# Kernel optimization log

Hardware: AMD Instinct MI355X
Metric: run time of the kernel (lower is better)

## Reference

```python
import jax, jax.numpy as jnp
import numpy as np

IM_H, IM_W = 32, 32
HEADS, HEAD_DIM = 8, 32
IN_DIM = 256
OUT_DIM = 256
N = IM_H * IM_W


def _relative_indices(h, w):
    # replicate torch meshgrid('ij') + flatten logic
    gy, gx = np.meshgrid(np.arange(h), np.arange(w), indexing='ij')
    pos = np.stack([gy.reshape(-1), gx.reshape(-1)])  # (2, n)
    rel = pos[:, :, None] - pos[:, None, :]           # (2, n, n)
    r0 = (rel[0] + (h - 1)) * (2 * w - 1)
    r1 = rel[1] + (w - 1)
    return (r0 + r1).reshape(-1)                      # (n*n,)

_REL_IDX = jnp.asarray(_relative_indices(IM_H, IM_W), dtype=jnp.int32)


def setup_inputs() -> dict:
    key = jax.random.key(0)
    ks = jax.random.split(key, 8)
    d_inner = HEADS * HEAD_DIM
    x = jax.random.normal(ks[0], (16, N, IN_DIM), dtype=jnp.float32)
    Wq = jax.random.normal(ks[1], (IN_DIM, d_inner), dtype=jnp.float32) / np.sqrt(IN_DIM)
    Wk = jax.random.normal(ks[2], (IN_DIM, d_inner), dtype=jnp.float32) / np.sqrt(IN_DIM)
    Wv = jax.random.normal(ks[3], (IN_DIM, d_inner), dtype=jnp.float32) / np.sqrt(IN_DIM)
    bias_table = jax.random.normal(ks[4], ((2 * IM_H - 1) * (2 * IM_W - 1), HEADS), dtype=jnp.float32)
    Wo = jax.random.normal(ks[5], (d_inner, OUT_DIM), dtype=jnp.float32) / np.sqrt(d_inner)
    bo = jax.random.normal(ks[6], (OUT_DIM,), dtype=jnp.float32) * 0.01
    return {"x": x, "Wq": Wq, "Wk": Wk, "Wv": Wv, "bias_table": bias_table, "Wo": Wo, "bo": bo}


def reference(x, Wq, Wk, Wv, bias_table, Wo, bo):
    b, n, _ = x.shape
    scale = HEAD_DIM ** (-0.5)
    # QKV projections -> [b, h, n, d]
    def proj(W):
        return (x @ W).reshape(b, n, HEADS, HEAD_DIM).transpose(0, 2, 1, 3)
    Q, K, V = proj(Wq), proj(Wk), proj(Wv)
    # gathered relative position bias -> [1, h, n, n]
    bias = bias_table[_REL_IDX].reshape(n, n, HEADS).transpose(2, 0, 1)[None]
    scores = jnp.einsum('bhnd,bhmd->bhnm', Q, K) * scale + bias
    attn = jax.nn.softmax(scores, axis=-1)
    out = jnp.einsum('bhnm,bhmd->bhnd', attn, V)
    out = out.transpose(0, 2, 1, 3).reshape(b, n, HEADS * HEAD_DIM)
    return out @ Wo + bo  # dropout is identity in eval mode
```

## Files before the change

### kernel.cpp

```cpp
#include <hip/hip_runtime.h>


using f32x4  = __attribute__((ext_vector_type(4))) float;
using bf16x8 = __attribute__((ext_vector_type(8))) short;

__device__ __forceinline__ short f2bf(float f) {
  union { float f; unsigned u; } v; v.f = f;
  return (short)((v.u + 0x7FFFu + ((v.u >> 16) & 1u)) >> 16);
}
__device__ __forceinline__ f32x4 mfma_k32(bf16x8 a, bf16x8 b, f32x4 c) {
  return __builtin_amdgcn_mfma_f32_16x16x32_bf16(a, b, c, 0, 0, 0);
}
__device__ __forceinline__ int cvt_pk_bf16(float lo, float hi) {
  int r;
  asm("v_cvt_pk_bf16_f32 %0, %1, %2" : "=v"(r) : "v"(lo), "v"(hi));
  return r;
}
__device__ __forceinline__ f32x4 ldb(const float* __restrict__ row, int p) {
  f32x4 v;
  v[0] = row[p]; v[1] = row[p - 1]; v[2] = row[p - 2]; v[3] = row[p - 3];
  return v;
}

#define CSQ 0.25500526817f

__global__ __launch_bounds__(256) void k_prep(const float* __restrict__ Wq,
    const float* __restrict__ Wk, const float* __restrict__ Wv,
    const float* __restrict__ Wo, short* __restrict__ WT,
    const float* __restrict__ bt, float* __restrict__ Tg) {
  int bx = blockIdx.x;
  if (bx < 1024) {
    int wid = bx >> 8, n = bx & 255, k = threadIdx.x;
    const float* W = wid == 0 ? Wq : wid == 1 ? Wk : wid == 2 ? Wv : Wo;
    WT[wid * 65536 + n * 256 + k] = f2bf(W[k * 256 + n]);
  } else {
    int idx = (bx - 1024) * 256 + threadIdx.x;
    int h = idx >> 12, i = idx & 4095;
    if (i < 3969) Tg[idx] = bt[i * 8 + h] * 1.4426950408889634f;
  }
}

__global__ __launch_bounds__(256) void k_qkv(const float* __restrict__ x,
    const short* __restrict__ WT,
    short* __restrict__ Q, short* __restrict__ K, short* __restrict__ Vt) {
  __shared__ short Wlds[2][4096];
  char* lbase = (char*)Wlds;
  const int tid = threadIdx.x;
  const int w = tid >> 6, l = tid & 63, lr = l & 15, lg = l >> 4;
  const int m0 = blockIdx.x * 64;
  const int wi = blockIdx.y;
  const char* Wb = (const char*)(WT + wi * 65536);
  const float* xrow = x + (size_t)(m0 + w * 16 + lr) * 256;
  bf16x8 af[8];
  #pragma unroll
  for (int kc = 0; kc < 8; ++kc) {
    float4 a = *reinterpret_cast<const float4*>(xrow + kc * 32 + lg * 8);
    float4 c = *reinterpret_cast<const float4*>(xrow + kc * 32 + lg * 8 + 4);
    union { int i4[4]; bf16x8 v; } u;
    u.i4[0] = cvt_pk_bf16(a.x, a.y);
    u.i4[1] = cvt_pk_bf16(a.z, a.w);
    u.i4[2] = cvt_pk_bf16(c.x, c.y);
    u.i4[3] = cvt_pk_bf16(c.z, c.w);
    af[kc] = u.v;
  }
  const int Lb0 = tid * 16, Lb1 = 4096 + tid * 16;
  const int P0 = Lb0 ^ (((Lb0 >> 9) & 7) << 4);
  const int P1 = Lb1 ^ (((Lb1 >> 9) & 7) << 4);
  int rdo[8];
  #pragma unroll
  for (int kc = 0; kc < 8; ++kc) {
    int Lg = lr * 512 + kc * 64 + lg * 16;
    rdo[kc] = Lg ^ ((lr & 7) << 4);
  }
  {
    int4 s0 = *reinterpret_cast<const int4*>(Wb + Lb0);
    int4 s1 = *reinterpret_cast<const int4*>(Wb + Lb1);
    *reinterpret_cast<int4*>(lbase + P0) = s0;
    *reinterpret_cast<int4*>(lbase + P1) = s1;
  }
  __syncthreads();
  #pragma unroll 2
  for (int nt = 0; nt < 16; ++nt) {
    const int cur = nt & 1, nxt = cur ^ 1;
    int4 t0, t1;
    if (nt < 15) {
      t0 = *reinterpret_cast<const int4*>(Wb + (nt + 1) * 8192 + Lb0);
      t1 = *reinterpret_cast<const int4*>(Wb + (nt + 1) * 8192 + Lb1);
    }
    f32x4 acc = {0.f, 0.f, 0.f, 0.f};
    #pragma unroll
    for (int kc = 0; kc < 8; ++kc) {
      bf16x8 bfr = *reinterpret_cast<const bf16x8*>(lbase + cur * 8192 + rdo[kc]);
      acc = mfma_k32(af[kc], bfr, acc);
    }
    int colb = nt * 16 + lr;
    int h = colb >> 5, d = colb & 31;
    if (wi == 2) {
      int m = m0 + w * 16 + lg * 4;
      int b = m >> 10, n0 = m & 1023;
      int js = n0 >> 5;
      int lgv = (n0 & 15) >> 2, hi = (n0 >> 4) & 1;
      int jp = lgv * 8 + hi * 4;
      short4 vv;
      vv.x = f2bf(acc[0]); vv.y = f2bf(acc[1]);
      vv.z = f2bf(acc[2]); vv.w = f2bf(acc[3]);
      *reinterpret_cast<short4*>(
          &Vt[(((size_t)(b * 8 + h) * 32 + js) << 10) + d * 32 + jp]) = vv;
    } else {
      #pragma unroll
      for (int r = 0; r < 4; ++r) {
        int m = m0 + w * 16 + lg * 4 + r;
        int b = m >> 10, n = m & 1023;
        short val = (wi == 0) ? f2bf(acc[r] * CSQ) : f2bf(acc[r]);
        if (wi == 0)
          Q[((size_t)(b * 8 + h) * 1024 + n) * 32 + d] = val;
        else
          K[((size_t)(b * 8 + h) * 1024 + n) * 32 + d] = val;
      }
    }
    if (nt < 15) {
      *reinterpret_cast<int4*>(lbase + nxt * 8192 + P0) = t0;
      *reinterpret_cast<int4*>(lbase + nxt * 8192 + P1) = t1;
    }
    __syncthreads();
  }
}

__global__ __launch_bounds__(512) void k_attn(const short* __restrict__ Q,
    const short* __restrict__ K, const short* __restrict__ Vt,
    const float* __restrict__ Tg, short* __restrict__ aout) {
  __shared__ char smraw[18432];
  float* Tlds = (float*)smraw;
  auto mO  = (float(*)[4][4][64])smraw;
  auto mls = (float(*)[2][64])(smraw + 16384);
  const int tid = threadIdx.x, bid = blockIdx.x;
  const int h = bid & 7, qt = (bid >> 3) & 7, b = bid >> 6;
  const float* Th = Tg + (h << 12);
  for (int t = tid; t < 3969; t += 512) Tlds[t] = Th[t];
  __syncthreads();
  const int wg = tid >> 6, l = tid & 63, lr = l & 15, lg = l >> 4;
  const int w = wg & 3, jh = wg >> 2;
  const size_t hoff = (size_t)(b * 8 + h) << 15;
  const short* Qh = Q + hoff;
  const short* Kh = K + hoff;
  const short* Vh = Vt + hoff;
  const int ita = qt * 4 + w;
  const int i0a = ita * 16;
  const int i0b = i0a + 512;
  const int yia = ita >> 1;
  const int pbase = ((ita & 1) << 4) + lr - lg * 4 + 31;
  bf16x8 qfa = *reinterpret_cast<const bf16x8*>(&Qh[(i0a + lr) * 32 + lg * 8]);
  bf16x8 qfb = *reinterpret_cast<const bf16x8*>(&Qh[(i0b + lr) * 32 + lg * 8]);
  f32x4 oa0 = {0.f,0.f,0.f,0.f}, oa1 = {0.f,0.f,0.f,0.f};
  f32x4 ob0 = {0.f,0.f,0.f,0.f}, ob1 = {0.f,0.f,0.f,0.f};
  float lsa = 0.f, lsb = 0.f;
  const int koff0 = lr * 32 + lg * 8, koff1 = (16 + lr) * 32 + lg * 8;
  const int js0 = jh * 16, jsE = js0 + 16;
  bf16x8 kf0 = *reinterpret_cast<const bf16x8*>(&Kh[(js0 << 10) + koff0]);
  bf16x8 kf1 = *reinterpret_cast<const bf16x8*>(&Kh[(js0 << 10) + koff1]);
  bf16x8 vf0 = *reinterpret_cast<const bf16x8*>(&Vh[(js0 << 10) + koff0]);
  bf16x8 vf1 = *reinterpret_cast<const bf16x8*>(&Vh[(js0 << 10) + koff1]);
  #pragma unroll 2
  for (int js = js0; js < jsE; ++js) {
    const int jn = (js + 1 < jsE) ? js + 1 : js;
    bf16x8 nkf0 = *reinterpret_cast<const bf16x8*>(&Kh[(jn << 10) + koff0]);
    bf16x8 nkf1 = *reinterpret_cast<const bf16x8*>(&Kh[(jn << 10) + koff1]);
    bf16x8 nvf0 = *reinterpret_cast<const bf16x8*>(&Vh[(jn << 10) + koff0]);
    bf16x8 nvf1 = *reinterpret_cast<const bf16x8*>(&Vh[(jn << 10) + koff1]);
    const float* TrowA = &Tlds[(yia - js + 31) * 63];
    f32x4 bA0 = ldb(TrowA, pbase);
    f32x4 bA1 = ldb(TrowA, pbase - 16);
    f32x4 bB0 = ldb(TrowA + 1008, pbase);
    f32x4 bB1 = ldb(TrowA + 1008, pbase - 16);
    f32x4 sa0 = mfma_k32(kf0, qfa, bA0);
    f32x4 sa1 = mfma_k32(kf1, qfa, bA1);
    f32x4 sb0 = mfma_k32(kf0, qfb, bB0);
    f32x4 sb1 = mfma_k32(kf1, qfb, bB1);
    float pa0[4], pa1[4], pb0[4], pb1[4];
    #pragma unroll
    for (int r = 0; r < 4; ++r) {
      pa0[r] = __builtin_amdgcn_exp2f(sa0[r]);
      pa1[r] = __builtin_amdgcn_exp2f(sa1[r]);
      pb0[r] = __builtin_amdgcn_exp2f(sb0[r]);
      pb1[r] = __builtin_amdgcn_exp2f(sb1[r]);
      lsa += pa0[r] + pa1[r];
      lsb += pb0[r] + pb1[r];
    }
    union { int i4[4]; bf16x8 v; } pka, pkb;
    pka.i4[0] = cvt_pk_bf16(pa0[0], pa0[1]);
    pka.i4[1] = cvt_pk_bf16(pa0[2], pa0[3]);
    pka.i4[2] = cvt_pk_bf16(pa1[0], pa1[1]);
    pka.i4[3] = cvt_pk_bf16(pa1[2], pa1[3]);
    pkb.i4[0] = cvt_pk_bf16(pb0[0], pb0[1]);
    pkb.i4[1] = cvt_pk_bf16(pb0[2], pb0[3]);
    pkb.i4[2] = cvt_pk_bf16(pb1[0], pb1[1]);
    pkb.i4[3] = cvt_pk_bf16(pb1[2], pb1[3]);
    oa0 = mfma_k32(pka.v, vf0, oa0);
    oa1 = mfma_k32(pka.v, vf1, oa1);
    ob0 = mfma_k32(pkb.v, vf0, ob0);
    ob1 = mfma_k32(pkb.v, vf1, ob1);
    kf0 = nkf0; kf1 = nkf1; vf0 = nvf0; vf1 = nvf1;
  }
  __syncthreads();
  if (jh == 1) {
    #pragma unroll
    for (int r = 0; r < 4; ++r) {
      mO[w][0][r][l] = oa0[r];
      mO[w][1][r][l] = oa1[r];
      mO[w][2][r][l] = ob0[r];
      mO[w][3][r][l] = ob1[r];
    }
    mls[w][0][l] = lsa;
    mls[w][1][l] = lsb;
  }
  __syncthreads();
  if (jh == 0) {
    #pragma unroll
    for (int r = 0; r < 4; ++r) {
      oa0[r] += mO[w][0][r][l];
      oa1[r] += mO[w][1][r][l];
      ob0[r] += mO[w][2][r][l];
      ob1[r] += mO[w][3][r][l];
    }
    lsa += mls[w][0][l];
    lsb += mls[w][1][l];
    {
      float s = lsa + __shfl_xor(lsa, 16);
      s += __shfl_xor(s, 32);
      float inv = 1.0f / s;
      #pragma unroll
      for (int r = 0; r < 4; ++r) {
        float invr = __shfl(inv, lg * 4 + r);
        int n = i0a + lg * 4 + r;
        size_t base = ((size_t)b << 18) + (size_t)n * 256 + h * 32;
        aout[base + lr]      = f2bf(oa0[r] * invr);
        aout[base + 16 + lr] = f2bf(oa1[r] * invr);
      }
      s = lsb + __shfl_xor(lsb, 16);
      s += __shfl_xor(s, 32);
      inv = 1.0f / s;
      #pragma unroll
      for (int r = 0; r < 4; ++r) {
        float invr = __shfl(inv, lg * 4 + r);
        int n = i0b + lg * 4 + r;
        size_t base = ((size_t)b << 18) + (size_t)n * 256 + h * 32;
        aout[base + lr]      = f2bf(ob0[r] * invr);
        aout[base + 16 + lr] = f2bf(ob1[r] * invr);
      }
    }
  }
}

__global__ __launch_bounds__(256) void k_outproj(const short* __restrict__ aout,
    const short* __restrict__ WoT, const float* __restrict__ bo,
    float* __restrict__ out) {
  __shared__ short Wlds[2][4096];
  char* lbase = (char*)Wlds;
  const int tid = threadIdx.x;
  const int w = tid >> 6, l = tid & 63, lr = l & 15, lg = l >> 4;
  const int m0 = blockIdx.x * 64;
  const char* Wb = (const char*)WoT;
  const short* arow = aout + (size_t)(m0 + w * 16 + lr) * 256;
  bf16x8 af[8];
  #pragma unroll
  for (int kc = 0; kc < 8; ++kc)
    af[kc] = *reinterpret_cast<const bf16x8*>(arow + kc * 32 + lg * 8);
  const int Lb0 = tid * 16, Lb1 = 4096 + tid * 16;
  const int P0 = Lb0 ^ (((Lb0 >> 9) & 7) << 4);
  const int P1 = Lb1 ^ (((Lb1 >> 9) & 7) << 4);
  int rdo[8];
  #pragma unroll
  for (int kc = 0; kc < 8; ++kc) {
    int Lg = lr * 512 + kc * 64 + lg * 16;
    rdo[kc] = Lg ^ ((lr & 7) << 4);
  }
  {
    int4 s0 = *reinterpret_cast<const int4*>(Wb + Lb0);
    int4 s1 = *reinterpret_cast<const int4*>(Wb + Lb1);
    *reinterpret_cast<int4*>(lbase + P0) = s0;
    *reinterpret_cast<int4*>(lbase + P1) = s1;
  }
  __syncthreads();
  #pragma unroll 2
  for (int nt = 0; nt < 16; ++nt) {
    const int cur = nt & 1, nxt = cur ^ 1;
    int4 t0, t1;
    if (nt < 15) {
      t0 = *reinterpret_cast<const int4*>(Wb + (nt + 1) * 8192 + Lb0);
      t1 = *reinterpret_cast<const int4*>(Wb + (nt + 1) * 8192 + Lb1);
    }
    f32x4 acc = {0.f, 0.f, 0.f, 0.f};
    #pragma unroll
    for (int kc = 0; kc < 8; ++kc) {
      bf16x8 bfr = *reinterpret_cast<const bf16x8*>(lbase + cur * 8192 + rdo[kc]);
      acc = mfma_k32(af[kc], bfr, acc);
    }
    int colb = nt * 16 + lr;
    float bias = bo[colb];
    #pragma unroll
    for (int r = 0; r < 4; ++r) {
      int m = m0 + w * 16 + lg * 4 + r;
      out[(size_t)m * 256 + colb] = acc[r] + bias;
    }
    if (nt < 15) {
      *reinterpret_cast<int4*>(lbase + nxt * 8192 + P0) = t0;
      *reinterpret_cast<int4*>(lbase + nxt * 8192 + P1) = t1;
    }
    __syncthreads();
  }
}

extern "C" void kernel_launch(void* const* d_in, const int* in_sizes, int n_in,
                              void* d_out, int out_size, void* d_ws, size_t ws_size,
                              hipStream_t stream) {
  const float* x  = (const float*)d_in[0];
  const float* Wq = (const float*)d_in[1];
  const float* Wk = (const float*)d_in[2];
  const float* Wv = (const float*)d_in[3];
  const float* bt = (const float*)d_in[4];
  const float* Wo = (const float*)d_in[5];
  const float* bo = (const float*)d_in[6];
  float* out = (float*)d_out;
  char* ws = (char*)d_ws;
  short* WT   = (short*)ws;
  short* Qs   = (short*)(ws + 512 * 1024);
  short* Ks   = Qs + 4194304;
  short* Vts  = Ks + 4194304;
  short* aout = Vts + 4194304;
  float* Tg   = (float*)(ws + 512 * 1024 + 4ull * 8388608);

  k_prep<<<1152, 256, 0, stream>>>(Wq, Wk, Wv, Wo, WT, bt, Tg);
  k_qkv<<<dim3(256, 3), 256, 0, stream>>>(x, WT, Qs, Ks, Vts);
  k_attn<<<1024, 512, 0, stream>>>(Qs, Ks, Vts, Tg, aout);
  k_outproj<<<256, 256, 0, stream>>>(aout, WT + 3 * 65536, bo, out);
}
```

Baseline: 77.98 us.

## Tile weight transpose, deepen K/V prefetch, split out-projection columns

The weight transpose in the prep kernel now goes through an LDS tile with vectorized float4 loads and short4 stores, replacing the strided per-element transpose that used 1024 blocks. The attention loop prefetches K/V fragments two iterations ahead instead of one, to hide more global-load latency at the cost of extra registers. The output projection grid is split across two column halves, doubling the block count so the GPU is better filled, while each block reloads the same activation rows.

Result: faster. 75.32 us (-3.4%).

```diff
diff --git a/kernel.cpp b/kernel.cpp
--- a/kernel.cpp
+++ b/kernel.cpp
@@ -29,12 +29,36 @@
     const float* __restrict__ Wo, short* __restrict__ WT,
     const float* __restrict__ bt, float* __restrict__ Tg) {
   int bx = blockIdx.x;
-  if (bx < 1024) {
-    int wid = bx >> 8, n = bx & 255, k = threadIdx.x;
+  if (bx < 64) {
+    __shared__ float tile[64][65];
+    int wid = bx >> 4, t = bx & 15;
+    int ro0 = (t & 3) * 64, co0 = (t >> 2) * 64;
     const float* W = wid == 0 ? Wq : wid == 1 ? Wk : wid == 2 ? Wv : Wo;
-    WT[wid * 65536 + n * 256 + k] = f2bf(W[k * 256 + n]);
+    int tr = threadIdx.x >> 4, tc = threadIdx.x & 15;
+    #pragma unroll
+    for (int c = 0; c < 4; ++c) {
+      int row = c * 16 + tr;
+      float4 v = *reinterpret_cast<const float4*>(
+          &W[(ro0 + row) * 256 + co0 + tc * 4]);
+      tile[row][tc * 4 + 0] = v.x;
+      tile[row][tc * 4 + 1] = v.y;
+      tile[row][tc * 4 + 2] = v.z;
+      tile[row][tc * 4 + 3] = v.w;
+    }
+    __syncthreads();
+    #pragma unroll
+    for (int c = 0; c < 4; ++c) {
+      int orow = c * 16 + tr;
+      short4 s;
+      s.x = f2bf(tile[tc * 4 + 0][orow]);
+      s.y = f2bf(tile[tc * 4 + 1][orow]);
+      s.z = f2bf(tile[tc * 4 + 2][orow]);
+      s.w = f2bf(tile[tc * 4 + 3][orow]);
+      *reinterpret_cast<short4*>(
+          &WT[wid * 65536 + (co0 + orow) * 256 + ro0 + tc * 4]) = s;
+    }
   } else {
-    int idx = (bx - 1024) * 256 + threadIdx.x;
+    int idx = (bx - 64) * 256 + threadIdx.x;
     int h = idx >> 12, i = idx & 4095;
     if (i < 3969) Tg[idx] = bt[i * 8 + h] * 1.4426950408889634f;
   }
@@ -156,26 +180,32 @@
   float lsa = 0.f, lsb = 0.f;
   const int koff0 = lr * 32 + lg * 8, koff1 = (16 + lr) * 32 + lg * 8;
   const int js0 = jh * 16, jsE = js0 + 16;
-  bf16x8 kf0 = *reinterpret_cast<const bf16x8*>(&Kh[(js0 << 10) + koff0]);
-  bf16x8 kf1 = *reinterpret_cast<const bf16x8*>(&Kh[(js0 << 10) + koff1]);
-  bf16x8 vf0 = *reinterpret_cast<const bf16x8*>(&Vh[(js0 << 10) + koff0]);
-  bf16x8 vf1 = *reinterpret_cast<const bf16x8*>(&Vh[(js0 << 10) + koff1]);
+  bf16x8 kA0 = *reinterpret_cast<const bf16x8*>(&Kh[(js0 << 10) + koff0]);
+  bf16x8 kA1 = *reinterpret_cast<const bf16x8*>(&Kh[(js0 << 10) + koff1]);
+  bf16x8 vA0 = *reinterpret_cast<const bf16x8*>(&Vh[(js0 << 10) + koff0]);
+  bf16x8 vA1 = *reinterpret_cast<const bf16x8*>(&Vh[(js0 << 10) + koff1]);
+  bf16x8 kB0 = *reinterpret_cast<const bf16x8*>(&Kh[((js0 + 1) << 10) + koff0]);
+  bf16x8 kB1 = *reinterpret_cast<const bf16x8*>(&Kh[((js0 + 1) << 10) + koff1]);
+  bf16x8 vB0 = *reinterpret_cast<const bf16x8*>(&Vh[((js0 + 1) << 10) + koff0]);
+  bf16x8 vB1 = *reinterpret_cast<const bf16x8*>(&Vh[((js0 + 1) << 10) + koff1]);
   #pragma unroll 2
-  for (int js = js0; js < jsE; ++js) {
-    const int jn = (js + 1 < jsE) ? js + 1 : js;
-    bf16x8 nkf0 = *reinterpret_cast<const bf16x8*>(&Kh[(jn << 10) + koff0]);
-    bf16x8 nkf1 = *reinterpret_cast<const bf16x8*>(&Kh[(jn << 10) + koff1]);
-    bf16x8 nvf0 = *reinterpret_cast<const bf16x8*>(&Vh[(jn << 10) + koff0]);
-    bf16x8 nvf1 = *reinterpret_cast<const bf16x8*>(&Vh[(jn << 10) + koff1]);
+  for (int t = 0; t < 16; ++t) {
+    const int js = js0 + t;
+    int jn = js + 2;
+    if (jn >= jsE) jn = jsE - 1;
+    bf16x8 nk0 = *reinterpret_cast<const bf16x8*>(&Kh[(jn << 10) + koff0]);
+    bf16x8 nk1 = *reinterpret_cast<const bf16x8*>(&Kh[(jn << 10) + koff1]);
+    bf16x8 nv0 = *reinterpret_cast<const bf16x8*>(&Vh[(jn << 10) + koff0]);
+    bf16x8 nv1 = *reinterpret_cast<const bf16x8*>(&Vh[(jn << 10) + koff1]);
     const float* TrowA = &Tlds[(yia - js + 31) * 63];
     f32x4 bA0 = ldb(TrowA, pbase);
     f32x4 bA1 = ldb(TrowA, pbase - 16);
     f32x4 bB0 = ldb(TrowA + 1008, pbase);
     f32x4 bB1 = ldb(TrowA + 1008, pbase - 16);
-    f32x4 sa0 = mfma_k32(kf0, qfa, bA0);
-    f32x4 sa1 = mfma_k32(kf1, qfa, bA1);
-    f32x4 sb0 = mfma_k32(kf0, qfb, bB0);
-    f32x4 sb1 = mfma_k32(kf1, qfb, bB1);
+    f32x4 sa0 = mfma_k32(kA0, qfa, bA0);
+    f32x4 sa1 = mfma_k32(kA1, qfa, bA1);
+    f32x4 sb0 = mfma_k32(kA0, qfb, bB0);
+    f32x4 sb1 = mfma_k32(kA1, qfb, bB1);
     float pa0[4], pa1[4], pb0[4], pb1[4];
     #pragma unroll
     for (int r = 0; r < 4; ++r) {
@@ -195,11 +225,12 @@
     pkb.i4[1] = cvt_pk_bf16(pb0[2], pb0[3]);
     pkb.i4[2] = cvt_pk_bf16(pb1[0], pb1[1]);
     pkb.i4[3] = cvt_pk_bf16(pb1[2], pb1[3]);
-    oa0 = mfma_k32(pka.v, vf0, oa0);
-    oa1 = mfma_k32(pka.v, vf1, oa1);
-    ob0 = mfma_k32(pkb.v, vf0, ob0);
-    ob1 = mfma_k32(pkb.v, vf1, ob1);
-    kf0 = nkf0; kf1 = nkf1; vf0 = nvf0; vf1 = nvf1;
+    oa0 = mfma_k32(pka.v, vA0, oa0);
+    oa1 = mfma_k32(pka.v, vA1, oa1);
+    ob0 = mfma_k32(pkb.v, vA0, ob0);
+    ob1 = mfma_k32(pkb.v, vA1, ob1);
+    kA0 = kB0; kA1 = kB1; vA0 = vB0; vA1 = vB1;
+    kB0 = nk0; kB1 = nk1; vB0 = nv0; vB1 = nv1;
   }
   __syncthreads();
   if (jh == 1) {
@@ -259,7 +290,8 @@
   const int tid = threadIdx.x;
   const int w = tid >> 6, l = tid & 63, lr = l & 15, lg = l >> 4;
   const int m0 = blockIdx.x * 64;
-  const char* Wb = (const char*)WoT;
+  const int nt0 = blockIdx.y * 8;
+  const char* Wb = (const char*)WoT + nt0 * 8192;
   const short* arow = aout + (size_t)(m0 + w * 16 + lr) * 256;
   bf16x8 af[8];
   #pragma unroll
@@ -282,12 +314,12 @@
   }
   __syncthreads();
   #pragma unroll 2
-  for (int nt = 0; nt < 16; ++nt) {
-    const int cur = nt & 1, nxt = cur ^ 1;
+  for (int t = 0; t < 8; ++t) {
+    const int cur = t & 1, nxt = cur ^ 1;
     int4 t0, t1;
-    if (nt < 15) {
-      t0 = *reinterpret_cast<const int4*>(Wb + (nt + 1) * 8192 + Lb0);
-      t1 = *reinterpret_cast<const int4*>(Wb + (nt + 1) * 8192 + Lb1);
+    if (t < 7) {
+      t0 = *reinterpret_cast<const int4*>(Wb + (t + 1) * 8192 + Lb0);
+      t1 = *reinterpret_cast<const int4*>(Wb + (t + 1) * 8192 + Lb1);
     }
     f32x4 acc = {0.f, 0.f, 0.f, 0.f};
     #pragma unroll
@@ -295,14 +327,14 @@
       bf16x8 bfr = *reinterpret_cast<const bf16x8*>(lbase + cur * 8192 + rdo[kc]);
       acc = mfma_k32(af[kc], bfr, acc);
     }
-    int colb = nt * 16 + lr;
+    int colb = (nt0 + t) * 16 + lr;
     float bias = bo[colb];
     #pragma unroll
     for (int r = 0; r < 4; ++r) {
       int m = m0 + w * 16 + lg * 4 + r;
       out[(size_t)m * 256 + colb] = acc[r] + bias;
     }
-    if (nt < 15) {
+    if (t < 7) {
       *reinterpret_cast<int4*>(lbase + nxt * 8192 + P0) = t0;
       *reinterpret_cast<int4*>(lbase + nxt * 8192 + P1) = t1;
     }
@@ -329,8 +361,8 @@
   short* aout = Vts + 4194304;
   float* Tg   = (float*)(ws + 512 * 1024 + 4ull * 8388608);
 
-  k_prep<<<1152, 256, 0, stream>>>(Wq, Wk, Wv, Wo, WT, bt, Tg);
+  k_prep<<<192, 256, 0, stream>>>(Wq, Wk, Wv, Wo, WT, bt, Tg);
   k_qkv<<<dim3(256, 3), 256, 0, stream>>>(x, WT, Qs, Ks, Vts);
   k_attn<<<1024, 512, 0, stream>>>(Qs, Ks, Vts, Tg, aout);
-  k_outproj<<<256, 256, 0, stream>>>(aout, WT + 3 * 65536, bo, out);
-}
+  k_outproj<<<dim3(256, 2), 256, 0, stream>>>(aout, WT + 3 * 65536, bo, out);
+}
```
